# Kernel optimization log

Hardware: AMD Instinct MI355X
Metric: run time of the kernel (lower is better)

The kernel has to match this reference:

```python
import jax, jax.numpy as jnp
import numpy as np

K_OUTLIER = 16   # decomposition_topk default k
Q = 127.0        # int8 symmetric quant scale


def _quantize(mat):
    # per-row abs-max symmetric quantization; torch .to(int8) truncates toward
    # zero, which matches XLA's float->int convert semantics.
    mmax = jnp.max(jnp.abs(mat), axis=-1)                      # [...,]
    q = (mat * (Q / mmax)[..., None]).astype(jnp.int8)
    return q, mmax


def setup_inputs() -> dict:
    key = jax.random.key(0)
    k1, k2, k3 = jax.random.split(key, 3)
    B, I, O = 4096, 2048, 2048
    x = jax.random.normal(k1, (B, I), jnp.float32)
    weight = jax.random.normal(k2, (O, I), jnp.float32) * 0.02  # nn.Linear convention [out, in]
    bias = jax.random.normal(k3, (O,), jnp.float32) * 0.02
    return {"x": x, "weight": weight, "bias": bias}


def reference(x, weight, bias):
    # --- weight-side prep (done once in __init__ in the torch module) ---
    col_max = jnp.max(jnp.abs(weight), axis=0)                 # [I] abs-max per input column
    idx = jax.lax.top_k(col_max, K_OUTLIER)[1]                 # [k] outlier input columns
    w_unq = weight[:, idx].T                                   # [k, O] fp outlier weights
    w0 = weight.at[:, idx].set(0.0)                            # zero outlier columns
    w_q, w_max = _quantize(w0)                                 # int8 [O, I], fp [O]

    # --- activation side ---
    x_unq = x[:, idx]                                          # [B, k]
    x1 = x.at[:, idx].set(0.0)
    x_q, x_max = _quantize(x1)                                 # int8 [B, I], fp [B]

    # int8 matmul accumulated in int32 (MatMulInteger), then dequantize
    res_q_i32 = jnp.matmul(x_q.astype(jnp.int32), w_q.T.astype(jnp.int32))  # [B, O]
    mx = x_max[:, None] * w_max[None, :]                       # outer product of row/col maxes
    res_q = (res_q_i32.astype(jnp.float32) / (Q * Q)).astype(jnp.float16).astype(jnp.float32) * mx

    # fp outlier path + bias
    res_unq = x_unq @ w_unq + bias                             # [B, O]
    return res_q + res_unq
```

## Files before the change

kernel.cpp:

```cpp
#include <hip/hip_runtime.h>
#include <hip/hip_fp16.h>
#include <stdint.h>

#define I_DIM 2048
#define O_DIM 2048
#define B_DIM 4096
#define KOUT 16

typedef int i32x4 __attribute__((ext_vector_type(4)));
typedef int i32x16 __attribute__((ext_vector_type(16)));
typedef float f32x4 __attribute__((ext_vector_type(4)));
typedef float f32x16 __attribute__((ext_vector_type(16)));
typedef _Float16 f16x8 __attribute__((ext_vector_type(8)));

#define TO_LDS(p) ((__attribute__((address_space(3))) void*)(p))
#define TO_GLB(p) ((const __attribute__((address_space(1))) void*)(p))

__global__ void colmax_kernel(const float* __restrict__ W, float* __restrict__ cmp) {
  int j = blockIdx.x * 256 + threadIdx.x;
  int i0 = blockIdx.y * 64;
  float m = 0.0f;
  const float* p = W + (size_t)i0 * I_DIM + j;
#pragma unroll 8
  for (int i = 0; i < 64; ++i)
    m = fmaxf(m, fabsf(p[(size_t)i * I_DIM]));
  cmp[blockIdx.y * I_DIM + j] = m;
}

__global__ void topk_kernel(const float* __restrict__ cmp, int* __restrict__ idx,
                            float* __restrict__ keep) {
  int t = threadIdx.x;
  float v[8];
#pragma unroll
  for (int u = 0; u < 8; ++u) v[u] = 0.0f;
  for (int rc = 0; rc < 32; ++rc) {
    const float* row = cmp + rc * I_DIM;
#pragma unroll
    for (int u = 0; u < 8; ++u) v[u] = fmaxf(v[u], row[u * 256 + t]);
  }
  for (int j = t; j < I_DIM; j += 256) keep[j] = 1.0f;
  __shared__ float wm_[4];
  __shared__ int wi_[4];
  __shared__ int sel;
  for (int k = 0; k < KOUT; ++k) {
    float m = v[0]; int mi = 0;
#pragma unroll
    for (int u = 1; u < 8; ++u) if (v[u] > m) { m = v[u]; mi = u; }
    int gi = mi * 256 + t;
#pragma unroll
    for (int s = 32; s; s >>= 1) {
      float om = __shfl_down(m, s);
      int oi = __shfl_down(gi, s);
      if (om > m) { m = om; gi = oi; }
    }
    if ((t & 63) == 0) { wm_[t >> 6] = m; wi_[t >> 6] = gi; }
    __syncthreads();
    if (t == 0) {
      float bm = wm_[0]; int bi = wi_[0];
      for (int w2 = 1; w2 < 4; ++w2) if (wm_[w2] > bm) { bm = wm_[w2]; bi = wi_[w2]; }
      idx[k] = bi; keep[bi] = 0.0f; sel = bi;
    }
    __syncthreads();
    if (t == (sel & 255)) v[sel >> 8] = -1.0f;
  }
}

__global__ __launch_bounds__(256) void quant_kernel(
    const float* __restrict__ X, const float* __restrict__ W,
    const float* __restrict__ keep, const int* __restrict__ idx,
    signed char* __restrict__ xq, signed char* __restrict__ wq,
    float* __restrict__ xmax, float* __restrict__ wmax,
    _Float16* __restrict__ xunqh,
    _Float16* __restrict__ wunqh) {
  int b = blockIdx.x;
  int t = threadIdx.x;
  bool isW = b < O_DIM;
  int r = isW ? b : (b - O_DIM);
  const float* src = isW ? (W + (size_t)r * I_DIM) : (X + (size_t)r * I_DIM);
  const float4* s4 = (const float4*)src;
  const float4* k4 = (const float4*)keep;
  float4 v0 = s4[t * 2], v1 = s4[t * 2 + 1];
  float4 k0 = k4[t * 2], k1 = k4[t * 2 + 1];
  v0.x *= k0.x; v0.y *= k0.y; v0.z *= k0.z; v0.w *= k0.w;
  v1.x *= k1.x; v1.y *= k1.y; v1.z *= k1.z; v1.w *= k1.w;
  float m = fmaxf(fmaxf(fmaxf(fabsf(v0.x), fabsf(v0.y)), fmaxf(fabsf(v0.z), fabsf(v0.w))),
                  fmaxf(fmaxf(fabsf(v1.x), fabsf(v1.y)), fmaxf(fabsf(v1.z), fabsf(v1.w))));
#pragma unroll
  for (int s = 32; s; s >>= 1) m = fmaxf(m, __shfl_xor(m, s));
  __shared__ float red[4];
  if ((t & 63) == 0) red[t >> 6] = m;
  __syncthreads();
  m = fmaxf(fmaxf(red[0], red[1]), fmaxf(red[2], red[3]));
  float sc = 127.0f / m;
  unsigned p0 = (unsigned char)(signed char)(int)(v0.x * sc)
              | ((unsigned)(unsigned char)(signed char)(int)(v0.y * sc) << 8)
              | ((unsigned)(unsigned char)(signed char)(int)(v0.z * sc) << 16)
              | ((unsigned)(unsigned char)(signed char)(int)(v0.w * sc) << 24);
  unsigned p1 = (unsigned char)(signed char)(int)(v1.x * sc)
              | ((unsigned)(unsigned char)(signed char)(int)(v1.y * sc) << 8)
              | ((unsigned)(unsigned char)(signed char)(int)(v1.z * sc) << 16)
              | ((unsigned)(unsigned char)(signed char)(int)(v1.w * sc) << 24);
  uint2* qout = (uint2*)(isW ? (wq + (size_t)r * I_DIM) : (xq + (size_t)r * I_DIM));
  qout[t] = make_uint2(p0, p1);
  if (t == 0) { if (isW) wmax[r] = m; else xmax[r] = m; }
  if (t < KOUT) {
    float ov = src[idx[t]];
    _Float16* u = isW ? (wunqh + (size_t)r * KOUT) : (xunqh + (size_t)r * KOUT);
    u[t] = (_Float16)ov;
  }
}

__global__ __launch_bounds__(256) void gemm_kernel(
    const signed char* __restrict__ Aq,
    const signed char* __restrict__ Bq,
    const float* __restrict__ xmaxg,
    const float* __restrict__ wmaxg,
    const _Float16* __restrict__ xunqh,
    const _Float16* __restrict__ wunqh,
    const float* __restrict__ biasg,
    float* __restrict__ out) {
  constexpr int N = O_DIM, K = I_DIM;
  __shared__ __align__(16) signed char smem[65536];

  const int tid = threadIdx.x;
  const int lane = tid & 63;
  const int wave = tid >> 6;
  const int h = lane >> 5;
  const int ln31 = lane & 31;
  const int wm = (wave & 1) * 64;
  const int wn = (wave >> 1) * 64;
  const int m0 = blockIdx.y * 128;
  const int n0 = blockIdx.x * 128;

  const signed char* srcA[4];
  const signed char* srcB[4];
#pragma unroll
  for (int s = 0; s < 4; ++s) {
    int f = (s * 4 + wave) * 64 + lane;
    int r = f >> 3;
    int g = (f & 7) ^ (r & 7);
    srcA[s] = Aq + (size_t)(m0 + r) * K + g * 16;
    srcB[s] = Bq + (size_t)(n0 + r) * K + g * 16;
  }

  const int rA0 = wm + ln31, rA1 = rA0 + 32;
  const int rB0 = wn + ln31, rB1 = rB0 + 32;
  const int oA0 = rA0 * 128, sA0 = rA0 & 7;
  const int oA1 = rA1 * 128, sA1 = rA1 & 7;
  const int oB0 = rB0 * 128, sB0 = rB0 & 7;
  const int oB1 = rB1 * 128, sB1 = rB1 & 7;

  f16x8 afh[2], bfh[2];
#pragma unroll
  for (int i = 0; i < 2; ++i)
    afh[i] = *(const f16x8*)(xunqh + (size_t)(m0 + wm + i * 32 + ln31) * KOUT + h * 8);
#pragma unroll
  for (int j = 0; j < 2; ++j)
    bfh[j] = *(const f16x8*)(wunqh + (size_t)(n0 + wn + j * 32 + ln31) * KOUT + h * 8);

  i32x16 acc[2][2] = {};

#pragma unroll
  for (int s = 0; s < 4; ++s) {
    __builtin_amdgcn_global_load_lds(TO_GLB(srcA[s]), TO_LDS(smem + (s * 4 + wave) * 1024), 16, 0, 0);
    __builtin_amdgcn_global_load_lds(TO_GLB(srcB[s]), TO_LDS(smem + 16384 + (s * 4 + wave) * 1024), 16, 0, 0);
  }
  __syncthreads();

  for (int it = 0; it < K / 128; ++it) {
    const int cur = (it & 1) * 32768;
    const int nxt = cur ^ 32768;
    if (it + 1 < K / 128) {
      int kt = (it + 1) * 128;
#pragma unroll
      for (int s = 0; s < 4; ++s) {
        __builtin_amdgcn_global_load_lds(TO_GLB(srcA[s] + kt), TO_LDS(smem + nxt + (s * 4 + wave) * 1024), 16, 0, 0);
        __builtin_amdgcn_global_load_lds(TO_GLB(srcB[s] + kt), TO_LDS(smem + nxt + 16384 + (s * 4 + wave) * 1024), 16, 0, 0);
      }
    }
    const signed char* As = smem + cur;
    const signed char* Bs = smem + cur + 16384;
#pragma unroll
    for (int st = 0; st < 4; ++st) {
      int lc = st * 2 + h;
      i32x4 a0 = *(const i32x4*)(As + oA0 + ((lc ^ sA0) << 4));
      i32x4 a1 = *(const i32x4*)(As + oA1 + ((lc ^ sA1) << 4));
      i32x4 b0 = *(const i32x4*)(Bs + oB0 + ((lc ^ sB0) << 4));
      i32x4 b1 = *(const i32x4*)(Bs + oB1 + ((lc ^ sB1) << 4));
      acc[0][0] = __builtin_amdgcn_mfma_i32_32x32x32_i8(a0, b0, acc[0][0], 0, 0, 0);
      acc[0][1] = __builtin_amdgcn_mfma_i32_32x32x32_i8(a0, b1, acc[0][1], 0, 0, 0);
      acc[1][0] = __builtin_amdgcn_mfma_i32_32x32x32_i8(a1, b0, acc[1][0], 0, 0, 0);
      acc[1][1] = __builtin_amdgcn_mfma_i32_32x32x32_i8(a1, b1, acc[1][1], 0, 0, 0);
    }
    __syncthreads();
  }

  const float recip = 1.0f / 16129.0f;
#pragma unroll
  for (int i = 0; i < 2; ++i) {
#pragma unroll
    for (int j = 0; j < 2; ++j) {
      int col = n0 + wn + j * 32 + ln31;
      float wmv = wmaxg[col];
      float bv = biasg[col];
      f32x16 c;
#pragma unroll
      for (int g = 0; g < 4; ++g) {
        int rbase = m0 + wm + i * 32 + g * 8 + h * 4;
        f32x4 xmv = *(const f32x4*)(xmaxg + rbase);
#pragma unroll
        for (int r = 0; r < 4; ++r) {
          float v = (float)acc[i][j][g * 4 + r] * recip;
          v = __half2float(__float2half(v));
          c[g * 4 + r] = v * (xmv[r] * wmv) + bv;
        }
      }
      c = __builtin_amdgcn_mfma_f32_32x32x16_f16(afh[i], bfh[j], c, 0, 0, 0);
#pragma unroll
      for (int g = 0; g < 4; ++g) {
        int rbase = m0 + wm + i * 32 + g * 8 + h * 4;
#pragma unroll
        for (int r = 0; r < 4; ++r)
          out[(size_t)(rbase + r) * N + col] = c[g * 4 + r];
      }
    }
  }
}

extern "C" void kernel_launch(void* const* d_in, const int* in_sizes, int n_in,
                              void* d_out, int out_size, void* d_ws, size_t ws_size,
                              hipStream_t stream) {
  const float* x    = (const float*)d_in[0];
  const float* w    = (const float*)d_in[1];
  const float* bias = (const float*)d_in[2];
  float* out = (float*)d_out;
  char* ws = (char*)d_ws;

  float* cm_part   = (float*)(ws + 0);
  int* idx         = (int*)(ws + 262144);
  float* keep      = (float*)(ws + 262272);
  float* w_max     = (float*)(ws + 270464);
  float* x_max     = (float*)(ws + 278656);
  _Float16* x_unqh = (_Float16*)(ws + 295040);
  _Float16* w_unqh = (_Float16*)(ws + 426112);
  signed char* w_q = (signed char*)(ws + 491648);
  signed char* x_q = (signed char*)(ws + 4685952);

  colmax_kernel<<<dim3(8, 32), 256, 0, stream>>>(w, cm_part);
  topk_kernel<<<1, 256, 0, stream>>>(cm_part, idx, keep);
  quant_kernel<<<O_DIM + B_DIM, 256, 0, stream>>>(x, w, keep, idx, x_q, w_q,
                                                  x_max, w_max, x_unqh, w_unqh);
  gemm_kernel<<<dim3(O_DIM / 128, B_DIM / 128), 256, 0, stream>>>(
      x_q, w_q, x_max, w_max, x_unqh, w_unqh, bias, out);
}
```

Baseline: 151.8 us.

## Enlarge GEMM tile to 128x256 with K-step 64 and two blocks per CU

The int8 GEMM now uses 128x256 output tiles, with each wave owning a 128x64 slab (4x2 MFMA accumulators). The K step shrinks from 128 to 64 and the shared-memory swizzle changes, cutting double-buffered LDS from 64KB to 48KB, and launch bounds now request two blocks per CU. The aim is more MFMA reuse per LDS fragment load and better occupancy, at the cost of more accumulator registers and more loop iterations and barriers. The column-max and top-k prep kernels are also tweaked: fewer partial rows and vectorized float4 reads.

```diff
diff --git a/kernel.cpp b/kernel.cpp
--- a/kernel.cpp
+++ b/kernel.cpp
@@ -18,11 +18,11 @@
 
 __global__ void colmax_kernel(const float* __restrict__ W, float* __restrict__ cmp) {
   int j = blockIdx.x * 256 + threadIdx.x;
-  int i0 = blockIdx.y * 64;
+  int i0 = blockIdx.y * 128;
   float m = 0.0f;
   const float* p = W + (size_t)i0 * I_DIM + j;
 #pragma unroll 8
-  for (int i = 0; i < 64; ++i)
+  for (int i = 0; i < 128; ++i)
     m = fmaxf(m, fabsf(p[(size_t)i * I_DIM]));
   cmp[blockIdx.y * I_DIM + j] = m;
 }
@@ -33,10 +33,13 @@
   float v[8];
 #pragma unroll
   for (int u = 0; u < 8; ++u) v[u] = 0.0f;
-  for (int rc = 0; rc < 32; ++rc) {
-    const float* row = cmp + rc * I_DIM;
-#pragma unroll
-    for (int u = 0; u < 8; ++u) v[u] = fmaxf(v[u], row[u * 256 + t]);
+  for (int rc = 0; rc < 16; ++rc) {
+    const float4* row = (const float4*)(cmp + rc * I_DIM);
+    float4 a4 = row[t * 2], b4 = row[t * 2 + 1];
+    v[0] = fmaxf(v[0], a4.x); v[1] = fmaxf(v[1], a4.y);
+    v[2] = fmaxf(v[2], a4.z); v[3] = fmaxf(v[3], a4.w);
+    v[4] = fmaxf(v[4], b4.x); v[5] = fmaxf(v[5], b4.y);
+    v[6] = fmaxf(v[6], b4.z); v[7] = fmaxf(v[7], b4.w);
   }
   for (int j = t; j < I_DIM; j += 256) keep[j] = 1.0f;
   __shared__ float wm_[4];
@@ -46,7 +49,7 @@
     float m = v[0]; int mi = 0;
 #pragma unroll
     for (int u = 1; u < 8; ++u) if (v[u] > m) { m = v[u]; mi = u; }
-    int gi = mi * 256 + t;
+    int gi = t * 8 + mi;
 #pragma unroll
     for (int s = 32; s; s >>= 1) {
       float om = __shfl_down(m, s);
@@ -61,7 +64,7 @@
       idx[k] = bi; keep[bi] = 0.0f; sel = bi;
     }
     __syncthreads();
-    if (t == (sel & 255)) v[sel >> 8] = -1.0f;
+    if (t == (sel >> 3)) v[sel & 7] = -1.0f;
   }
 }
 
@@ -110,7 +113,7 @@
   }
 }
 
-__global__ __launch_bounds__(256) void gemm_kernel(
+__global__ __launch_bounds__(256, 2) void gemm_kernel(
     const signed char* __restrict__ Aq,
     const signed char* __restrict__ Bq,
     const float* __restrict__ xmaxg,
@@ -120,84 +123,97 @@
     const float* __restrict__ biasg,
     float* __restrict__ out) {
   constexpr int N = O_DIM, K = I_DIM;
-  __shared__ __align__(16) signed char smem[65536];
+  __shared__ __align__(16) signed char smem[49152];
 
   const int tid = threadIdx.x;
   const int lane = tid & 63;
   const int wave = tid >> 6;
   const int h = lane >> 5;
   const int ln31 = lane & 31;
-  const int wm = (wave & 1) * 64;
-  const int wn = (wave >> 1) * 64;
+  const int wn = wave * 64;
   const int m0 = blockIdx.y * 128;
-  const int n0 = blockIdx.x * 128;
-
-  const signed char* srcA[4];
-  const signed char* srcB[4];
-#pragma unroll
-  for (int s = 0; s < 4; ++s) {
-    int f = (s * 4 + wave) * 64 + lane;
-    int r = f >> 3;
-    int g = (f & 7) ^ (r & 7);
-    srcA[s] = Aq + (size_t)(m0 + r) * K + g * 16;
-    srcB[s] = Bq + (size_t)(n0 + r) * K + g * 16;
-  }
-
-  const int rA0 = wm + ln31, rA1 = rA0 + 32;
-  const int rB0 = wn + ln31, rB1 = rB0 + 32;
-  const int oA0 = rA0 * 128, sA0 = rA0 & 7;
-  const int oA1 = rA1 * 128, sA1 = rA1 & 7;
-  const int oB0 = rB0 * 128, sB0 = rB0 & 7;
-  const int oB1 = rB1 * 128, sB1 = rB1 & 7;
-
-  f16x8 afh[2], bfh[2];
-#pragma unroll
-  for (int i = 0; i < 2; ++i)
-    afh[i] = *(const f16x8*)(xunqh + (size_t)(m0 + wm + i * 32 + ln31) * KOUT + h * 8);
+  const int n0 = blockIdx.x * 256;
+
+  const signed char* srcP[6];
+  int dstoff[6];
+#pragma unroll
+  for (int s = 0; s < 6; ++s) {
+    if (s < 2) {
+      int f = s * 256 + tid;
+      int r = f >> 2, p = f & 3;
+      int g = p ^ ((r ^ (r >> 2)) & 3);
+      srcP[s] = Aq + (size_t)(m0 + r) * K + g * 16;
+      dstoff[s] = s * 4096 + wave * 1024;
+    } else {
+      int f = (s - 2) * 256 + tid;
+      int r = f >> 2, p = f & 3;
+      int g = p ^ ((r ^ (r >> 2)) & 3);
+      srcP[s] = Bq + (size_t)(n0 + r) * K + g * 16;
+      dstoff[s] = 8192 + (s - 2) * 4096 + wave * 1024;
+    }
+  }
+
+  int oA[4], sA[4], oB[2], sB[2];
+#pragma unroll
+  for (int i = 0; i < 4; ++i) {
+    int r = i * 32 + ln31;
+    oA[i] = r * 64; sA[i] = (r ^ (r >> 2)) & 3;
+  }
+#pragma unroll
+  for (int j = 0; j < 2; ++j) {
+    int r = wn + j * 32 + ln31;
+    oB[j] = 8192 + r * 64; sB[j] = (r ^ (r >> 2)) & 3;
+  }
+
+  f16x8 afh[4], bfh[2];
+#pragma unroll
+  for (int i = 0; i < 4; ++i)
+    afh[i] = *(const f16x8*)(xunqh + (size_t)(m0 + i * 32 + ln31) * KOUT + h * 8);
 #pragma unroll
   for (int j = 0; j < 2; ++j)
     bfh[j] = *(const f16x8*)(wunqh + (size_t)(n0 + wn + j * 32 + ln31) * KOUT + h * 8);
 
-  i32x16 acc[2][2] = {};
-
-#pragma unroll
-  for (int s = 0; s < 4; ++s) {
-    __builtin_amdgcn_global_load_lds(TO_GLB(srcA[s]), TO_LDS(smem + (s * 4 + wave) * 1024), 16, 0, 0);
-    __builtin_amdgcn_global_load_lds(TO_GLB(srcB[s]), TO_LDS(smem + 16384 + (s * 4 + wave) * 1024), 16, 0, 0);
-  }
+  i32x16 acc[4][2] = {};
+
+#pragma unroll
+  for (int s = 0; s < 6; ++s)
+    __builtin_amdgcn_global_load_lds(TO_GLB(srcP[s]), TO_LDS(smem + dstoff[s]), 16, 0, 0);
   __syncthreads();
 
-  for (int it = 0; it < K / 128; ++it) {
-    const int cur = (it & 1) * 32768;
-    const int nxt = cur ^ 32768;
-    if (it + 1 < K / 128) {
-      int kt = (it + 1) * 128;
-#pragma unroll
-      for (int s = 0; s < 4; ++s) {
-        __builtin_amdgcn_global_load_lds(TO_GLB(srcA[s] + kt), TO_LDS(smem + nxt + (s * 4 + wave) * 1024), 16, 0, 0);
-        __builtin_amdgcn_global_load_lds(TO_GLB(srcB[s] + kt), TO_LDS(smem + nxt + 16384 + (s * 4 + wave) * 1024), 16, 0, 0);
-      }
-    }
-    const signed char* As = smem + cur;
-    const signed char* Bs = smem + cur + 16384;
-#pragma unroll
-    for (int st = 0; st < 4; ++st) {
+  for (int it = 0; it < K / 64; ++it) {
+    const int cur = (it & 1) * 24576;
+    const int nxt = cur ^ 24576;
+    if (it + 1 < K / 64) {
+      int kt = (it + 1) * 64;
+#pragma unroll
+      for (int s = 0; s < 6; ++s)
+        __builtin_amdgcn_global_load_lds(TO_GLB(srcP[s] + kt), TO_LDS(smem + nxt + dstoff[s]), 16, 0, 0);
+    }
+    const signed char* buf = smem + cur;
+#pragma unroll
+    for (int st = 0; st < 2; ++st) {
       int lc = st * 2 + h;
-      i32x4 a0 = *(const i32x4*)(As + oA0 + ((lc ^ sA0) << 4));
-      i32x4 a1 = *(const i32x4*)(As + oA1 + ((lc ^ sA1) << 4));
-      i32x4 b0 = *(const i32x4*)(Bs + oB0 + ((lc ^ sB0) << 4));
-      i32x4 b1 = *(const i32x4*)(Bs + oB1 + ((lc ^ sB1) << 4));
+      i32x4 a0 = *(const i32x4*)(buf + oA[0] + ((lc ^ sA[0]) << 4));
+      i32x4 a1 = *(const i32x4*)(buf + oA[1] + ((lc ^ sA[1]) << 4));
+      i32x4 a2 = *(const i32x4*)(buf + oA[2] + ((lc ^ sA[2]) << 4));
+      i32x4 a3 = *(const i32x4*)(buf + oA[3] + ((lc ^ sA[3]) << 4));
+      i32x4 b0 = *(const i32x4*)(buf + oB[0] + ((lc ^ sB[0]) << 4));
+      i32x4 b1 = *(const i32x4*)(buf + oB[1] + ((lc ^ sB[1]) << 4));
       acc[0][0] = __builtin_amdgcn_mfma_i32_32x32x32_i8(a0, b0, acc[0][0], 0, 0, 0);
       acc[0][1] = __builtin_amdgcn_mfma_i32_32x32x32_i8(a0, b1, acc[0][1], 0, 0, 0);
       acc[1][0] = __builtin_amdgcn_mfma_i32_32x32x32_i8(a1, b0, acc[1][0], 0, 0, 0);
       acc[1][1] = __builtin_amdgcn_mfma_i32_32x32x32_i8(a1, b1, acc[1][1], 0, 0, 0);
+      acc[2][0] = __builtin_amdgcn_mfma_i32_32x32x32_i8(a2, b0, acc[2][0], 0, 0, 0);
+      acc[2][1] = __builtin_amdgcn_mfma_i32_32x32x32_i8(a2, b1, acc[2][1], 0, 0, 0);
+      acc[3][0] = __builtin_amdgcn_mfma_i32_32x32x32_i8(a3, b0, acc[3][0], 0, 0, 0);
+      acc[3][1] = __builtin_amdgcn_mfma_i32_32x32x32_i8(a3, b1, acc[3][1], 0, 0, 0);
     }
     __syncthreads();
   }
 
   const float recip = 1.0f / 16129.0f;
 #pragma unroll
-  for (int i = 0; i < 2; ++i) {
+  for (int i = 0; i < 4; ++i) {
 #pragma unroll
     for (int j = 0; j < 2; ++j) {
       int col = n0 + wn + j * 32 + ln31;
@@ -206,7 +222,7 @@
       f32x16 c;
 #pragma unroll
       for (int g = 0; g < 4; ++g) {
-        int rbase = m0 + wm + i * 32 + g * 8 + h * 4;
+        int rbase = m0 + i * 32 + g * 8 + h * 4;
         f32x4 xmv = *(const f32x4*)(xmaxg + rbase);
 #pragma unroll
         for (int r = 0; r < 4; ++r) {
@@ -218,7 +234,7 @@
       c = __builtin_amdgcn_mfma_f32_32x32x16_f16(afh[i], bfh[j], c, 0, 0, 0);
 #pragma unroll
       for (int g = 0; g < 4; ++g) {
-        int rbase = m0 + wm + i * 32 + g * 8 + h * 4;
+        int rbase = m0 + i * 32 + g * 8 + h * 4;
 #pragma unroll
         for (int r = 0; r < 4; ++r)
           out[(size_t)(rbase + r) * N + col] = c[g * 4 + r];
@@ -237,19 +253,19 @@
   char* ws = (char*)d_ws;
 
   float* cm_part   = (float*)(ws + 0);
-  int* idx         = (int*)(ws + 262144);
-  float* keep      = (float*)(ws + 262272);
-  float* w_max     = (float*)(ws + 270464);
-  float* x_max     = (float*)(ws + 278656);
-  _Float16* x_unqh = (_Float16*)(ws + 295040);
-  _Float16* w_unqh = (_Float16*)(ws + 426112);
-  signed char* w_q = (signed char*)(ws + 491648);
-  signed char* x_q = (signed char*)(ws + 4685952);
-
-  colmax_kernel<<<dim3(8, 32), 256, 0, stream>>>(w, cm_part);
+  int* idx         = (int*)(ws + 131072);
+  float* keep      = (float*)(ws + 131200);
+  float* w_max     = (float*)(ws + 139392);
+  float* x_max     = (float*)(ws + 147584);
+  _Float16* x_unqh = (_Float16*)(ws + 163968);
+  _Float16* w_unqh = (_Float16*)(ws + 295040);
+  signed char* w_q = (signed char*)(ws + 360576);
+  signed char* x_q = (signed char*)(ws + 4554880);
+
+  colmax_kernel<<<dim3(8, 16), 256, 0, stream>>>(w, cm_part);
   topk_kernel<<<1, 256, 0, stream>>>(cm_part, idx, keep);
   quant_kernel<<<O_DIM + B_DIM, 256, 0, stream>>>(x, w, keep, idx, x_q, w_q,
                                                   x_max, w_max, x_unqh, w_unqh);
-  gemm_kernel<<<dim3(O_DIM / 128, B_DIM / 128), 256, 0, stream>>>(
+  gemm_kernel<<<dim3(O_DIM / 256, B_DIM / 128), 256, 0, stream>>>(
       x_q, w_q, x_max, w_max, x_unqh, w_unqh, bias, out);
 }
```

After: 163.4 us. 1.08x slower.
